# Performance work log

Measured on AMD Instinct MI355X. Metric: run time of the kernel, lower is better.

The kernel has to match this reference:

```python
import math
import jax, jax.numpy as jnp
import numpy as np

N_WL = 262144
T_REF = 273.15          # CONSTANTS.STANDARD_TEMPERATURE [K]
P_REF = 101325.0        # CONSTANTS.STANDARD_PRESSURE [Pa]
C_LIGHT = 2.99792458e8  # CONSTANTS.SPEED_OF_LIGHT
K_B = 1.380649e-23      # CONSTANTS.BOLTZMANN
N_AVO = 6.02214076e23   # CONSTANTS.AVOGADRO

# hard-coded line database: [center_wl, strength, width, temp_exp]; rows 0-2 O3, 3-5 H2O, 6-9 CO2
LINES = np.array([
    [254.0, 1.15e-17, 2.0, 0.05], [280.0, 5e-18, 3.0, 0.04], [310.0, 1.9e-19, 2.5, 0.03],
    [940.0, 2.5e-23, 3.0, 0.4],  [1130.0, 8.2e-24, 2.5, 0.35], [1380.0, 1.8e-22, 4.0, 0.45],
    [1400.0, 3.5e-25, 3.0, 0.5], [1600.0, 7.8e-26, 2.5, 0.48], [2000.0, 4.2e-24, 4.0, 0.52],
    [2700.0, 1.2e-24, 3.5, 0.49]], dtype=np.float32)
MASS = np.array([48.0]*3 + [18.0]*3 + [44.0]*4, dtype=np.float32)


def setup_inputs() -> dict:
    key = jax.random.key(0)
    ks = jax.random.split(key, 8)
    inp = {
        'wavelengths': jnp.linspace(200.0, 3000.0, N_WL, dtype=jnp.float32),
        'temperature': jnp.float32(250.0),
        'pressure': jnp.float32(80000.0),
        'conc_o3': jnp.float32(1e-6),
        'conc_h2o': jnp.float32(1e-2),
        'conc_co2': jnp.float32(4e-4),
        'mix_w1': jax.random.normal(ks[0], (10, 64), jnp.float32) * 0.3,
        'mix_b1': jnp.zeros((64,), jnp.float32),
        'mix_w2': jax.random.normal(ks[1], (64, 64), jnp.float32) * 0.12,
        'mix_b2': jnp.zeros((64,), jnp.float32),
        'mix_w3': jax.random.normal(ks[2], (64, N_WL), jnp.float32) * 0.12,
        'mix_b3': jnp.zeros((N_WL,), jnp.float32),
        'cont_w1': jax.random.normal(ks[3], (5, 32), jnp.float32) * 0.4,
        'cont_b1': jnp.zeros((32,), jnp.float32),
        'cont_w2': jax.random.normal(ks[4], (32, N_WL), jnp.float32) * 0.17,
        'cont_b2': jnp.zeros((N_WL,), jnp.float32),
    }
    return inp


def _voigt(wl, nu0, gamma_L, gamma_D):
    # wl: [N]; nu0, gamma_L, gamma_D: [L] -> returns [L, N]
    sigma = gamma_D / (math.sqrt(2.0 * math.log(2.0)) + 1e-12)          # [L]
    x = (wl[None, :] - nu0[:, None]) / (sigma[:, None] + 1e-12)          # [L,N]
    y = (gamma_L / (sigma + 1e-12))[:, None]                             # [L,1]
    t = y - 1j * x
    s = jnp.abs(x) + y
    mask1 = s >= 15.0
    mask2 = (s < 15.0) & (jnp.abs(x) >= 5.5)
    w1 = (t * 0.5641896 / (0.5 + t ** 2)).real
    u = t ** 2
    w2 = (t * (1.410474 + u * 0.5641896) / (0.75 + u * (3.0 + u))).real
    w3 = (jnp.exp(-x ** 2) * jnp.cos(2.0 * x * y) / math.sqrt(math.pi)
          + 2.0 * y / math.pi * jnp.sin(x ** 2) / (x ** 2 + y ** 2 + 1e-10))
    result = jnp.where(mask1, w1, jnp.where(mask2, w2, w3))
    return result / (sigma[:, None] * math.sqrt(math.pi) + 1e-12)


def reference(wavelengths, temperature, pressure, conc_o3, conc_h2o, conc_co2,
              mix_w1, mix_b1, mix_w2, mix_b2, mix_w3, mix_b3,
              cont_w1, cont_b1, cont_w2, cont_b2):
    lines = jnp.asarray(LINES)
    mass = jnp.asarray(MASS)
    conc = jnp.stack([conc_o3, conc_o3, conc_o3,
                      conc_h2o, conc_h2o, conc_h2o,
                      conc_co2, conc_co2, conc_co2, conc_co2])          # [10]
    nu0, strength, width, temp_exp = lines[:, 0], lines[:, 1], lines[:, 2], lines[:, 3]
    strength_T = strength * (T_REF / (temperature + 1e-12)) ** temp_exp  # [10]
    gamma_L = width * (pressure / (P_REF + 1e-12)) * jnp.sqrt(T_REF / (temperature + 1e-12))
    gamma_D = nu0 / C_LIGHT * jnp.sqrt(2.0 * K_B * temperature * N_AVO / (mass + 1e-12))

    profiles = _voigt(wavelengths, nu0, gamma_L, gamma_D)                # [10,N]
    cross = jnp.sum((conc * strength_T)[:, None] * profiles, axis=0)     # [N]

    # continuum net: 5 -> 32 (SiLU) -> N (softplus)
    cont_feat = jnp.stack([temperature / (T_REF + 1e-12),
                           pressure / (P_REF + 1e-12),
                           conc_h2o,
                           jnp.float32(1.0), jnp.float32(0.0)])
    h = jax.nn.silu(cont_feat @ cont_w1 + cont_b1)
    continuum = jax.nn.softplus(h @ cont_w2 + cont_b2)
    cross = cross + continuum

    # line-mixing net: 10 -> 64 (SiLU) -> 64 (SiLU) -> N (sigmoid); dropout is eval-mode identity
    mix_feat = jnp.concatenate([jnp.stack([temperature / (T_REF + 1e-12),
                                           pressure / (P_REF + 1e-12)]),
                                cross[:8]])
    m = jax.nn.silu(mix_feat @ mix_w1 + mix_b1)
    m = jax.nn.silu(m @ mix_w2 + mix_b2)
    mixing = jax.nn.sigmoid(m @ mix_w3 + mix_b3)
    return cross * (1.0 + 0.1 * (mixing - 0.5))
```

## Files before the change

kernel.cpp:

```cpp
#include <hip/hip_runtime.h>
#include <math.h>

#define N_WL 262144

#define T_REF 273.15
#define P_REF 101325.0
#define C_LIGHT 299792458.0
#define K_B 1.380649e-23
#define N_AVO 6.02214076e+23

__constant__ float c_nu0[10]  = {254.0f, 280.0f, 310.0f, 940.0f, 1130.0f, 1380.0f, 1400.0f, 1600.0f, 2000.0f, 2700.0f};
__constant__ float c_str[10]  = {1.15e-17f, 5e-18f, 1.9e-19f, 2.5e-23f, 8.2e-24f, 1.8e-22f, 3.5e-25f, 7.8e-26f, 4.2e-24f, 1.2e-24f};
__constant__ float c_wid[10]  = {2.0f, 3.0f, 2.5f, 3.0f, 2.5f, 4.0f, 3.0f, 2.5f, 4.0f, 3.5f};
__constant__ float c_texp[10] = {0.05f, 0.04f, 0.03f, 0.4f, 0.35f, 0.45f, 0.5f, 0.48f, 0.52f, 0.49f};
__constant__ float c_mass[10] = {48.f, 48.f, 48.f, 18.f, 18.f, 18.f, 44.f, 44.f, 44.f, 44.f};
__constant__ int   c_cidx[10] = {0, 0, 0, 1, 1, 1, 2, 2, 2, 2};

#define WS_M2    0
#define WS_H     64
#define WS_NU0   96
#define WS_ISIG  106
#define WS_Y     116
#define WS_SCALE 126
#define WS_TOT   136

__device__ __forceinline__ float siluf(float x)     { return x / (1.0f + __expf(-x)); }
__device__ __forceinline__ float sigmoidf(float x)  { return 1.0f / (1.0f + __expf(-x)); }
__device__ __forceinline__ float softplusf(float x) { return fmaxf(x, 0.0f) + log1pf(expf(-fabsf(x))); }

__device__ __forceinline__ float voigt_w(float x, float y) {
    float ax = fabsf(x);
    float s  = ax + y;
    if (s >= 15.0f) {
        float ur = y * y - x * x;
        float ui = -2.0f * x * y;
        float dr = 0.5f + ur, di = ui;
        float nr = 0.5641896f * y, ni = 0.5641896f * (-x);
        float den = dr * dr + di * di;
        return (nr * dr + ni * di) / den;
    } else if (ax >= 5.5f) {
        float ur = y * y - x * x;
        float ui = -2.0f * x * y;
        float pr = 1.410474f + 0.5641896f * ur;
        float pi_ = 0.5641896f * ui;
        float tr = y, ti = -x;
        float nr = tr * pr - ti * pi_;
        float ni = tr * pi_ + ti * pr;
        float u2r = ur * ur - ui * ui;
        float u2i = 2.0f * ur * ui;
        float dr = 0.75f + 3.0f * ur + u2r;
        float di = 3.0f * ui + u2i;
        float den = dr * dr + di * di;
        return (nr * dr + ni * di) / den;
    } else {
        float x2 = x * x;
        return expf(-x2) * cosf(2.0f * x * y) * 0.5641895835477563f
             + (2.0f * y / 3.14159265358979f) * sinf(x2) / (x2 + y * y + 1e-10f);
    }
}

__global__ void GasAbs_setup_kernel(
    const float* __restrict__ wl,
    const float* __restrict__ Tp, const float* __restrict__ Pp,
    const float* __restrict__ o3, const float* __restrict__ h2o, const float* __restrict__ co2,
    const float* __restrict__ mix_w1, const float* __restrict__ mix_b1,
    const float* __restrict__ mix_w2, const float* __restrict__ mix_b2,
    const float* __restrict__ cont_w1, const float* __restrict__ cont_b1,
    const float* __restrict__ cont_w2, const float* __restrict__ cont_b2,
    float* __restrict__ ws)
{
    __shared__ float sp[WS_TOT];
    __shared__ float s_feat[10];
    __shared__ float s_m1[64];

    const int t = threadIdx.x;
    const double T = (double)Tp[0];
    const double P = (double)Pp[0];
    const float  cc[3] = {o3[0], h2o[0], co2[0]};

    if (t < 10) {
        double nu0 = (double)c_nu0[t];
        double sT  = (double)c_str[t] * pow(T_REF / (T + 1e-12), (double)c_texp[t]);
        double gL  = (double)c_wid[t] * (P / (P_REF + 1e-12)) * sqrt(T_REF / (T + 1e-12));
        double gD  = nu0 / C_LIGHT * sqrt(2.0 * K_B * T * N_AVO / ((double)c_mass[t] + 1e-12));
        double sig = gD / (sqrt(2.0 * log(2.0)) + 1e-12);
        sp[WS_NU0  + t] = (float)nu0;
        sp[WS_ISIG + t] = (float)(1.0 / (sig + 1e-12));
        sp[WS_Y    + t] = (float)(gL / (sig + 1e-12));
        sp[WS_SCALE+ t] = (float)((double)cc[c_cidx[t]] * sT / (sig * sqrt(M_PI) + 1e-12));
    }
    if (t < 32) {
        float cf[5];
        cf[0] = (float)(T / (T_REF + 1e-12));
        cf[1] = (float)(P / (P_REF + 1e-12));
        cf[2] = cc[1];
        cf[3] = 1.0f;
        cf[4] = 0.0f;
        float a = cont_b1[t];
        #pragma unroll
        for (int k = 0; k < 5; k++) a += cf[k] * cont_w1[k * 32 + t];
        sp[WS_H + t] = siluf(a);
    }
    __syncthreads();

    if (t < 8) {
        float w = wl[t];
        float c = cont_b2[t];
        #pragma unroll
        for (int j = 0; j < 32; j++) c += sp[WS_H + j] * cont_w2[(size_t)j * N_WL + t];
        float cross = softplusf(c);
        #pragma unroll
        for (int l = 0; l < 10; l++) {
            float x = (w - sp[WS_NU0 + l]) * sp[WS_ISIG + l];
            cross += sp[WS_SCALE + l] * voigt_w(x, sp[WS_Y + l]);
        }
        s_feat[2 + t] = cross;
    }
    if (t == 0) {
        s_feat[0] = (float)(T / (T_REF + 1e-12));
        s_feat[1] = (float)(P / (P_REF + 1e-12));
    }
    __syncthreads();

    {
        float a = mix_b1[t];
        #pragma unroll
        for (int k = 0; k < 10; k++) a += s_feat[k] * mix_w1[k * 64 + t];
        s_m1[t] = siluf(a);
    }
    __syncthreads();

    {
        float a = mix_b2[t];
        #pragma unroll
        for (int k = 0; k < 64; k++) a += s_m1[k] * mix_w2[k * 64 + t];
        sp[WS_M2 + t] = siluf(a);
    }
    __syncthreads();

    ws[t] = sp[t];
    if (t < WS_TOT - 64) ws[64 + t] = sp[64 + t];
}

__global__ __launch_bounds__(256) void GasAbs_main_kernel(
    const float* __restrict__ wl,
    const float* __restrict__ mix_w3, const float* __restrict__ mix_b3,
    const float* __restrict__ cont_w2, const float* __restrict__ cont_b2,
    const float* __restrict__ ws,
    float* __restrict__ out)
{
    __shared__ float sp[WS_TOT];
    const int t = threadIdx.x;
    if (t < WS_TOT) sp[t] = ws[t];
    __syncthreads();

    const int i = blockIdx.x * 256 + t;

    const float w = wl[i];

    float c = cont_b2[i];
    #pragma unroll
    for (int j = 0; j < 32; j++)
        c = fmaf(sp[WS_H + j], cont_w2[(size_t)j * N_WL + i], c);

    float cross = softplusf(c);

    #pragma unroll
    for (int l = 0; l < 10; l++) {
        const float x = (w - sp[WS_NU0 + l]) * sp[WS_ISIG + l];
        cross = fmaf(sp[WS_SCALE + l], voigt_w(x, sp[WS_Y + l]), cross);
    }

    float m = mix_b3[i];
    #pragma unroll
    for (int j = 0; j < 64; j++)
        m = fmaf(sp[WS_M2 + j], mix_w3[(size_t)j * N_WL + i], m);

    out[i] = cross * (0.95f + 0.1f * sigmoidf(m));
}

extern "C" void kernel_launch(void* const* d_in, const int* in_sizes, int n_in,
                              void* d_out, int out_size, void* d_ws, size_t ws_size,
                              hipStream_t stream) {
    const float* wl      = (const float*)d_in[0];
    const float* Tp      = (const float*)d_in[1];
    const float* Pp      = (const float*)d_in[2];
    const float* o3      = (const float*)d_in[3];
    const float* h2o     = (const float*)d_in[4];
    const float* co2     = (const float*)d_in[5];
    const float* mix_w1  = (const float*)d_in[6];
    const float* mix_b1  = (const float*)d_in[7];
    const float* mix_w2  = (const float*)d_in[8];
    const float* mix_b2  = (const float*)d_in[9];
    const float* mix_w3  = (const float*)d_in[10];
    const float* mix_b3  = (const float*)d_in[11];
    const float* cont_w1 = (const float*)d_in[12];
    const float* cont_b1 = (const float*)d_in[13];
    const float* cont_w2 = (const float*)d_in[14];
    const float* cont_b2 = (const float*)d_in[15];
    float* ws  = (float*)d_ws;
    float* out = (float*)d_out;

    GasAbs_setup_kernel<<<1, 64, 0, stream>>>(
        wl, Tp, Pp, o3, h2o, co2,
        mix_w1, mix_b1, mix_w2, mix_b2,
        cont_w1, cont_b1, cont_w2, cont_b2, ws);

    const int threads = 256;
    const int blocks  = N_WL / threads;
    GasAbs_main_kernel<<<blocks, threads, 0, stream>>>(
        wl, mix_w3, mix_b3, cont_w2, cont_b2, ws, out);
}
```

Measured before the change: 153.5 us.

## Fuse setup MLP into main kernel and vectorize with float4 per thread

Merges the single-block setup kernel into the main kernel, with each block redundantly computing the small MLP hidden layers and line parameters in shared memory. The main loop now processes four wavelengths per thread using float4 loads of the large weight matrices. This removes a kernel launch and the workspace round trip, and aims to raise bytes in flight per thread. The trade-off is redundant per-block setup work and a grid of only 256 blocks, which lowers occupancy.

```diff
diff --git a/kernel.cpp b/kernel.cpp
--- a/kernel.cpp
+++ b/kernel.cpp
@@ -15,14 +15,6 @@
 __constant__ float c_texp[10] = {0.05f, 0.04f, 0.03f, 0.4f, 0.35f, 0.45f, 0.5f, 0.48f, 0.52f, 0.49f};
 __constant__ float c_mass[10] = {48.f, 48.f, 48.f, 18.f, 18.f, 18.f, 44.f, 44.f, 44.f, 44.f};
 __constant__ int   c_cidx[10] = {0, 0, 0, 1, 1, 1, 2, 2, 2, 2};
-
-#define WS_M2    0
-#define WS_H     64
-#define WS_NU0   96
-#define WS_ISIG  106
-#define WS_Y     116
-#define WS_SCALE 126
-#define WS_TOT   136
 
 __device__ __forceinline__ float siluf(float x)     { return x / (1.0f + __expf(-x)); }
 __device__ __forceinline__ float sigmoidf(float x)  { return 1.0f / (1.0f + __expf(-x)); }
@@ -59,47 +51,52 @@
     }
 }
 
-__global__ void GasAbs_setup_kernel(
+__global__ __launch_bounds__(256) void GasAbs_fused_kernel(
     const float* __restrict__ wl,
     const float* __restrict__ Tp, const float* __restrict__ Pp,
     const float* __restrict__ o3, const float* __restrict__ h2o, const float* __restrict__ co2,
     const float* __restrict__ mix_w1, const float* __restrict__ mix_b1,
     const float* __restrict__ mix_w2, const float* __restrict__ mix_b2,
+    const float* __restrict__ mix_w3, const float* __restrict__ mix_b3,
     const float* __restrict__ cont_w1, const float* __restrict__ cont_b1,
     const float* __restrict__ cont_w2, const float* __restrict__ cont_b2,
-    float* __restrict__ ws)
+    float* __restrict__ out)
 {
-    __shared__ float sp[WS_TOT];
+    __shared__ float s_nu0[10], s_isig[10], s_y[10], s_scale[10];
+    __shared__ float s_h[32];
     __shared__ float s_feat[10];
     __shared__ float s_m1[64];
+    __shared__ float s_m2[64];
 
     const int t = threadIdx.x;
-    const double T = (double)Tp[0];
-    const double P = (double)Pp[0];
-    const float  cc[3] = {o3[0], h2o[0], co2[0]};
 
     if (t < 10) {
+        const double T = (double)Tp[0];
+        const double P = (double)Pp[0];
+        const float cc3[3] = {o3[0], h2o[0], co2[0]};
         double nu0 = (double)c_nu0[t];
         double sT  = (double)c_str[t] * pow(T_REF / (T + 1e-12), (double)c_texp[t]);
         double gL  = (double)c_wid[t] * (P / (P_REF + 1e-12)) * sqrt(T_REF / (T + 1e-12));
         double gD  = nu0 / C_LIGHT * sqrt(2.0 * K_B * T * N_AVO / ((double)c_mass[t] + 1e-12));
         double sig = gD / (sqrt(2.0 * log(2.0)) + 1e-12);
-        sp[WS_NU0  + t] = (float)nu0;
-        sp[WS_ISIG + t] = (float)(1.0 / (sig + 1e-12));
-        sp[WS_Y    + t] = (float)(gL / (sig + 1e-12));
-        sp[WS_SCALE+ t] = (float)((double)cc[c_cidx[t]] * sT / (sig * sqrt(M_PI) + 1e-12));
+        s_nu0[t]   = (float)nu0;
+        s_isig[t]  = (float)(1.0 / (sig + 1e-12));
+        s_y[t]     = (float)(gL / (sig + 1e-12));
+        s_scale[t] = (float)((double)cc3[c_cidx[t]] * sT / (sig * sqrt(M_PI) + 1e-12));
     }
     if (t < 32) {
+        const double T = (double)Tp[0];
+        const double P = (double)Pp[0];
         float cf[5];
         cf[0] = (float)(T / (T_REF + 1e-12));
         cf[1] = (float)(P / (P_REF + 1e-12));
-        cf[2] = cc[1];
+        cf[2] = h2o[0];
         cf[3] = 1.0f;
         cf[4] = 0.0f;
         float a = cont_b1[t];
         #pragma unroll
-        for (int k = 0; k < 5; k++) a += cf[k] * cont_w1[k * 32 + t];
-        sp[WS_H + t] = siluf(a);
+        for (int k = 0; k < 5; k++) a = fmaf(cf[k], cont_w1[k * 32 + t], a);
+        s_h[t] = siluf(a);
     }
     __syncthreads();
 
@@ -107,76 +104,85 @@
         float w = wl[t];
         float c = cont_b2[t];
         #pragma unroll
-        for (int j = 0; j < 32; j++) c += sp[WS_H + j] * cont_w2[(size_t)j * N_WL + t];
+        for (int j = 0; j < 32; j++) c = fmaf(s_h[j], cont_w2[(size_t)j * N_WL + t], c);
         float cross = softplusf(c);
         #pragma unroll
         for (int l = 0; l < 10; l++) {
-            float x = (w - sp[WS_NU0 + l]) * sp[WS_ISIG + l];
-            cross += sp[WS_SCALE + l] * voigt_w(x, sp[WS_Y + l]);
+            float x = (w - s_nu0[l]) * s_isig[l];
+            cross = fmaf(s_scale[l], voigt_w(x, s_y[l]), cross);
         }
         s_feat[2 + t] = cross;
     }
     if (t == 0) {
+        const double T = (double)Tp[0];
+        const double P = (double)Pp[0];
         s_feat[0] = (float)(T / (T_REF + 1e-12));
         s_feat[1] = (float)(P / (P_REF + 1e-12));
     }
     __syncthreads();
 
-    {
+    if (t < 64) {
         float a = mix_b1[t];
         #pragma unroll
-        for (int k = 0; k < 10; k++) a += s_feat[k] * mix_w1[k * 64 + t];
+        for (int k = 0; k < 10; k++) a = fmaf(s_feat[k], mix_w1[k * 64 + t], a);
         s_m1[t] = siluf(a);
     }
     __syncthreads();
 
-    {
+    if (t < 64) {
         float a = mix_b2[t];
         #pragma unroll
-        for (int k = 0; k < 64; k++) a += s_m1[k] * mix_w2[k * 64 + t];
-        sp[WS_M2 + t] = siluf(a);
-    }
-    __syncthreads();
-
-    ws[t] = sp[t];
-    if (t < WS_TOT - 64) ws[64 + t] = sp[64 + t];
-}
-
-__global__ __launch_bounds__(256) void GasAbs_main_kernel(
-    const float* __restrict__ wl,
-    const float* __restrict__ mix_w3, const float* __restrict__ mix_b3,
-    const float* __restrict__ cont_w2, const float* __restrict__ cont_b2,
-    const float* __restrict__ ws,
-    float* __restrict__ out)
-{
-    __shared__ float sp[WS_TOT];
-    const int t = threadIdx.x;
-    if (t < WS_TOT) sp[t] = ws[t];
-    __syncthreads();
-
-    const int i = blockIdx.x * 256 + t;
-
-    const float w = wl[i];
-
-    float c = cont_b2[i];
-    #pragma unroll
-    for (int j = 0; j < 32; j++)
-        c = fmaf(sp[WS_H + j], cont_w2[(size_t)j * N_WL + i], c);
-
-    float cross = softplusf(c);
+        for (int k = 0; k < 64; k++) a = fmaf(s_m1[k], mix_w2[k * 64 + t], a);
+        s_m2[t] = siluf(a);
+    }
+    __syncthreads();
+
+    const int i0 = (blockIdx.x * 256 + t) * 4;
+
+    const float4 w4 = *reinterpret_cast<const float4*>(wl + i0);
+
+    float4 ac = *reinterpret_cast<const float4*>(cont_b2 + i0);
+    #pragma unroll 16
+    for (int j = 0; j < 32; j++) {
+        const float hj = s_h[j];
+        const float4 v = *reinterpret_cast<const float4*>(cont_w2 + (size_t)j * N_WL + i0);
+        ac.x = fmaf(hj, v.x, ac.x);
+        ac.y = fmaf(hj, v.y, ac.y);
+        ac.z = fmaf(hj, v.z, ac.z);
+        ac.w = fmaf(hj, v.w, ac.w);
+    }
+
+    float cr0 = softplusf(ac.x);
+    float cr1 = softplusf(ac.y);
+    float cr2 = softplusf(ac.z);
+    float cr3 = softplusf(ac.w);
 
     #pragma unroll
     for (int l = 0; l < 10; l++) {
-        const float x = (w - sp[WS_NU0 + l]) * sp[WS_ISIG + l];
-        cross = fmaf(sp[WS_SCALE + l], voigt_w(x, sp[WS_Y + l]), cross);
-    }
-
-    float m = mix_b3[i];
-    #pragma unroll
-    for (int j = 0; j < 64; j++)
-        m = fmaf(sp[WS_M2 + j], mix_w3[(size_t)j * N_WL + i], m);
-
-    out[i] = cross * (0.95f + 0.1f * sigmoidf(m));
+        const float nu0 = s_nu0[l], isig = s_isig[l], yy = s_y[l], sc = s_scale[l];
+        cr0 = fmaf(sc, voigt_w((w4.x - nu0) * isig, yy), cr0);
+        cr1 = fmaf(sc, voigt_w((w4.y - nu0) * isig, yy), cr1);
+        cr2 = fmaf(sc, voigt_w((w4.z - nu0) * isig, yy), cr2);
+        cr3 = fmaf(sc, voigt_w((w4.w - nu0) * isig, yy), cr3);
+    }
+
+    float4 am = *reinterpret_cast<const float4*>(mix_b3 + i0);
+    #pragma unroll 16
+    for (int j = 0; j < 64; j++) {
+        const float mj = s_m2[j];
+        const float4 v = *reinterpret_cast<const float4*>(mix_w3 + (size_t)j * N_WL + i0);
+        am.x = fmaf(mj, v.x, am.x);
+        am.y = fmaf(mj, v.y, am.y);
+        am.z = fmaf(mj, v.z, am.z);
+        am.w = fmaf(mj, v.w, am.w);
+    }
+
+    float4 o;
+    o.x = cr0 * (0.95f + 0.1f * sigmoidf(am.x));
+    o.y = cr1 * (0.95f + 0.1f * sigmoidf(am.y));
+    o.z = cr2 * (0.95f + 0.1f * sigmoidf(am.z));
+    o.w = cr3 * (0.95f + 0.1f * sigmoidf(am.w));
+    *reinterpret_cast<float4*>(out + i0) = o;
 }
 
 extern "C" void kernel_launch(void* const* d_in, const int* in_sizes, int n_in,
@@ -198,16 +204,12 @@
     const float* cont_b1 = (const float*)d_in[13];
     const float* cont_w2 = (const float*)d_in[14];
     const float* cont_b2 = (const float*)d_in[15];
-    float* ws  = (float*)d_ws;
     float* out = (float*)d_out;
 
-    GasAbs_setup_kernel<<<1, 64, 0, stream>>>(
+    const int threads = 256;
+    const int blocks  = N_WL / (threads * 4);
+    GasAbs_fused_kernel<<<blocks, threads, 0, stream>>>(
         wl, Tp, Pp, o3, h2o, co2,
-        mix_w1, mix_b1, mix_w2, mix_b2,
-        cont_w1, cont_b1, cont_w2, cont_b2, ws);
-
-    const int threads = 256;
-    const int blocks  = N_WL / threads;
-    GasAbs_main_kernel<<<blocks, threads, 0, stream>>>(
-        wl, mix_w3, mix_b3, cont_w2, cont_b2, ws, out);
+        mix_w1, mix_b1, mix_w2, mix_b2, mix_w3, mix_b3,
+        cont_w1, cont_b1, cont_w2, cont_b2, out);
 }
```

Result: no change. 153.8 us (+0.2%).
